# Kernel tuning notes

Hardware: AMD Instinct MI355X
Metric: run time of the kernel (lower is better)

## Reference

```python
import jax, jax.numpy as jnp
import numpy as np

B, Q, K, H = 16, 512, 512, 64
DQ, DK, DV = 256, 256, 256
MASK_VAL = -1000000.0


def setup_inputs() -> dict:
    key = jax.random.key(0)
    ks = jax.random.split(key, 7)
    queries = jax.random.normal(ks[0], (B, Q, DQ), dtype=jnp.float32)
    keys = jax.random.normal(ks[1], (B, K, DK), dtype=jnp.float32)
    values = jax.random.normal(ks[2], (B, K, DV), dtype=jnp.float32)
    valid_lens = jax.random.randint(ks[3], (B,), 1, K + 1).astype(jnp.int32)
    # learned params (nn.Linear, bias=False): weight shape [out, in]
    Wq = jax.random.normal(ks[4], (H, DQ), dtype=jnp.float32) / np.sqrt(DQ)
    Wk = jax.random.normal(ks[5], (H, DK), dtype=jnp.float32) / np.sqrt(DK)
    wv = jax.random.normal(ks[6], (H,), dtype=jnp.float32) / np.sqrt(H)
    return {"queries": queries, "keys": keys, "values": values,
            "valid_lens": valid_lens, "Wq": Wq, "Wk": Wk, "wv": wv}


def reference(queries, keys, values, valid_lens, Wq, Wk, wv):
    q = jnp.einsum('bqd,hd->bqh', queries, Wq)          # [B,Q,H]
    k = jnp.einsum('bkd,hd->bkh', keys, Wk)             # [B,K,H]
    feats = jnp.tanh(q[:, :, None, :] + k[:, None, :, :])  # [B,Q,K,H]
    scores = jnp.einsum('bqkh,h->bqk', feats, wv)       # [B,Q,K]
    kmask = jnp.arange(K)[None, None, :] < valid_lens[:, None, None]
    scores = jnp.where(kmask, scores, MASK_VAL)
    attn = jax.nn.softmax(scores, axis=-1)              # [B,Q,K]
    return jnp.einsum('bqk,bkv->bqv', attn, values)     # [B,Q,DV]
```

## Files before the change

kernel.cpp:

```cpp
#include <hip/hip_runtime.h>
#include <math.h>

#if defined(__has_builtin)
#  if __has_builtin(__builtin_amdgcn_exp2f)
#    define EXP2F(x) __builtin_amdgcn_exp2f(x)
#  endif
#  if __has_builtin(__builtin_amdgcn_rcpf)
#    define RCPF(x) __builtin_amdgcn_rcpf(x)
#  endif
#endif
#ifndef EXP2F
#  define EXP2F(x) exp2f(x)
#endif
#ifndef RCPF
#  define RCPF(x) (1.0f/(x))
#endif

static constexpr int Bn = 16, QN = 512, KN = 512, Hn = 64, DV = 256, DIN = 256;
static constexpr int TQ = 8;
static constexpr float TWO_LOG2E = 2.8853900817779268f;
static constexpr float LOG2E     = 1.4426950408889634f;

__global__ __launch_bounds__(512) void proj_kernel(
    const float* __restrict__ queries, const float* __restrict__ keys,
    const float* __restrict__ Wq, const float* __restrict__ Wk,
    float* __restrict__ qeT, float* __restrict__ ekT)
{
  __shared__ __align__(16) float xs[64][132];
  int t = threadIdx.x;
  int blk = blockIdx.x;
  bool is_k = blk >= 128;
  int tile = blk & 127;
  const float* X = is_k ? keys : queries;
  const float* W = is_k ? Wk : Wq;
  int row0 = tile * 64;
  int lane = t & 63;
  int w8 = __builtin_amdgcn_readfirstlane(t >> 6);
  const float* Wb = W + (size_t)w8 * 8 * DIN;
  float acc[8];
  #pragma unroll
  for (int j = 0; j < 8; ++j) acc[j] = 0.f;

  #pragma unroll
  for (int kc = 0; kc < 2; ++kc) {
    __syncthreads();
    #pragma unroll
    for (int j = 0; j < 4; ++j) {
      int idx = t + 512 * j;
      int row = idx >> 5, c4 = idx & 31;
      *(float4*)&xs[row][c4 * 4] =
          *(const float4*)(X + (size_t)(row0 + row) * DIN + kc * 128 + c4 * 4);
    }
    __syncthreads();
    const float* Wc = Wb + kc * 128;
    #pragma unroll 4
    for (int kq = 0; kq < 32; ++kq) {
      float4 x4 = *(const float4*)&xs[lane][kq * 4];
      #pragma unroll
      for (int j = 0; j < 8; ++j) {
        float4 w4 = *(const float4*)(Wc + j * DIN + kq * 4);
        acc[j] += x4.x * w4.x + x4.y * w4.y + x4.z * w4.z + x4.w * w4.w;
      }
    }
  }
  int row = row0 + lane;
  int b = row >> 9, rk = row & (KN - 1);
  float* outp = is_k ? ekT : qeT;
  #pragma unroll
  for (int j = 0; j < 8; ++j)
    outp[((size_t)b * Hn + w8 * 8 + j) * KN + rk] = EXP2F(acc[j] * TWO_LOG2E);
}

__global__ __launch_bounds__(512) void attn_kernel(
    const float* __restrict__ qeT,
    const float* __restrict__ ekT,
    const float* __restrict__ values,
    const int*   __restrict__ valid_lens,
    const float* __restrict__ wv,
    float* __restrict__ out)
{
  __shared__ __align__(16) float pt[KN][12];
  __shared__ __align__(16) float pacc[3][TQ][DV];
  __shared__ float wsum[8][TQ];
  __shared__ float inv_s[TQ];

  int t = threadIdx.x;
  int b = blockIdx.x >> 6;
  int q0 = (blockIdx.x & 63) * TQ;
  int L = valid_lens[b];
  int lane = t & 63, wave = t >> 6;

  float S = 0.f;
  #pragma unroll
  for (int h = 0; h < Hn; ++h) S += wv[h];

  {
    int k = t;
    float sc[TQ];
    #pragma unroll
    for (int r = 0; r < TQ; ++r) sc[r] = S;
    if (k < L) {
      const float* qbase = qeT + (size_t)b * Hn * QN + q0;
      const float* kbase = ekT + (size_t)b * Hn * KN + k;
      #pragma unroll 2
      for (int h = 0; h < Hn; ++h) {
        float ek = kbase[(size_t)h * KN];
        const float* qp = qbase + (size_t)h * QN;
        float w2 = 2.0f * wv[h];
        #pragma unroll
        for (int r = 0; r < TQ; ++r) {
          float d = qp[r] * ek + 1.0f;
          sc[r] -= w2 * RCPF(d);
        }
      }
    }
    float p[TQ];
    #pragma unroll
    for (int r = 0; r < TQ; ++r) p[r] = (k < L) ? EXP2F(sc[r] * LOG2E) : 0.f;
    if (k < L) {
      *(float4*)&pt[k][0] = make_float4(p[0], p[1], p[2], p[3]);
      *(float4*)&pt[k][4] = make_float4(p[4], p[5], p[6], p[7]);
    }
    #pragma unroll
    for (int r = 0; r < TQ; ++r) {
      float s = p[r];
      #pragma unroll
      for (int off = 32; off > 0; off >>= 1) s += __shfl_xor(s, off, 64);
      if (lane == r) wsum[wave][r] = s;
    }
  }
  __syncthreads();
  if (t < TQ) {
    float s = 0.f;
    #pragma unroll
    for (int w = 0; w < 8; ++w) s += wsum[w][t];
    inv_s[t] = 1.0f / s;
  }
  __syncthreads();

  int p2 = t & 127, kq = t >> 7;
  int c = p2 * 2;
  int k0 = (L * kq) >> 2, k1 = (L * (kq + 1)) >> 2;
  float a0[TQ], a1[TQ];
  #pragma unroll
  for (int r = 0; r < TQ; ++r) { a0[r] = 0.f; a1[r] = 0.f; }
  const float* vb = values + (size_t)b * KN * DV + c;
  #pragma unroll 2
  for (int k = k0; k < k1; ++k) {
    float2 v2 = *(const float2*)(vb + (size_t)k * DV);
    float4 pa = *(const float4*)&pt[k][0];
    float4 pb = *(const float4*)&pt[k][4];
    a0[0] += pa.x * v2.x; a1[0] += pa.x * v2.y;
    a0[1] += pa.y * v2.x; a1[1] += pa.y * v2.y;
    a0[2] += pa.z * v2.x; a1[2] += pa.z * v2.y;
    a0[3] += pa.w * v2.x; a1[3] += pa.w * v2.y;
    a0[4] += pb.x * v2.x; a1[4] += pb.x * v2.y;
    a0[5] += pb.y * v2.x; a1[5] += pb.y * v2.y;
    a0[6] += pb.z * v2.x; a1[6] += pb.z * v2.y;
    a0[7] += pb.w * v2.x; a1[7] += pb.w * v2.y;
  }
  if (kq) {
    #pragma unroll
    for (int r = 0; r < TQ; ++r)
      *(float2*)&pacc[kq - 1][r][c] = make_float2(a0[r], a1[r]);
  }
  __syncthreads();
  if (kq == 0) {
    float* ob = out + ((size_t)b * QN + q0) * DV + c;
    #pragma unroll
    for (int r = 0; r < TQ; ++r) {
      float s0 = a0[r], s1 = a1[r];
      #pragma unroll
      for (int q = 0; q < 3; ++q) {
        float2 pp = *(const float2*)&pacc[q][r][c];
        s0 += pp.x; s1 += pp.y;
      }
      float iv = inv_s[r];
      *(float2*)(ob + (size_t)r * DV) = make_float2(s0 * iv, s1 * iv);
    }
  }
}

extern "C" void kernel_launch(void* const* d_in, const int* in_sizes, int n_in,
                              void* d_out, int out_size, void* d_ws, size_t ws_size,
                              hipStream_t stream) {
  const float* queries    = (const float*)d_in[0];
  const float* keys       = (const float*)d_in[1];
  const float* values     = (const float*)d_in[2];
  const int*   valid_lens = (const int*)d_in[3];
  const float* Wq         = (const float*)d_in[4];
  const float* Wk         = (const float*)d_in[5];
  const float* wv         = (const float*)d_in[6];
  float* out = (float*)d_out;

  float* qeT = (float*)d_ws;
  float* ekT = qeT + (size_t)Bn * Hn * QN;

  proj_kernel<<<256, 512, 0, stream>>>(queries, keys, Wq, Wk, qeT, ekT);
  attn_kernel<<<Bn * (QN / TQ), 512, 0, stream>>>(qeT, ekT, values,
                                                  valid_lens, wv, out);
}
```

Measured before the change: 150.3 us.

## Use MFMA projection and persistent longest-first attention task scheduling

Replaces the scalar projection with a bf16 split-precision (hi/lo three-MFMA) matrix-core kernel that writes queries in row-major layout. Adds an ordering kernel that sorts batches by valid length, and makes the attention kernel persistent, pulling tasks longest-first from an atomic counter to balance the uneven per-batch work. Query features are staged in LDS, and partial outputs are reduced with shared atomics into a single buffer. This adds an extra launch and atomic overhead, and slightly changes projection precision.

```diff
diff --git a/kernel.cpp b/kernel.cpp
--- a/kernel.cpp
+++ b/kernel.cpp
@@ -18,165 +18,231 @@
 
 static constexpr int Bn = 16, QN = 512, KN = 512, Hn = 64, DV = 256, DIN = 256;
 static constexpr int TQ = 8;
+static constexpr int NTASK = Bn * (QN / TQ);
 static constexpr float TWO_LOG2E = 2.8853900817779268f;
 static constexpr float LOG2E     = 1.4426950408889634f;
 
-__global__ __launch_bounds__(512) void proj_kernel(
+typedef __attribute__((ext_vector_type(8))) short short8;
+typedef __attribute__((ext_vector_type(4))) float f32x4;
+
+__device__ __forceinline__ short f2bf(float x) {
+  unsigned u = __builtin_bit_cast(unsigned, x);
+  u += 0x7FFF + ((u >> 16) & 1);
+  return (short)(u >> 16);
+}
+__device__ __forceinline__ float bf2f(short h) {
+  return __builtin_bit_cast(float, ((unsigned)(unsigned short)h) << 16);
+}
+
+__global__ __launch_bounds__(256) void proj_mfma(
     const float* __restrict__ queries, const float* __restrict__ keys,
     const float* __restrict__ Wq, const float* __restrict__ Wk,
-    float* __restrict__ qeT, float* __restrict__ ekT)
+    float* __restrict__ qe, float* __restrict__ ekT)
 {
-  __shared__ __align__(16) float xs[64][132];
   int t = threadIdx.x;
-  int blk = blockIdx.x;
-  bool is_k = blk >= 128;
-  int tile = blk & 127;
+  int lane = t & 63, wid = t >> 6;
+  bool is_k = blockIdx.x >= 128;
   const float* X = is_k ? keys : queries;
   const float* W = is_k ? Wk : Wq;
-  int row0 = tile * 64;
-  int lane = t & 63;
-  int w8 = __builtin_amdgcn_readfirstlane(t >> 6);
-  const float* Wb = W + (size_t)w8 * 8 * DIN;
-  float acc[8];
+  int m0 = (blockIdx.x & 127) * 64 + wid * 16;
+  int mr = lane & 15, quad = lane >> 4;
+  const float* xp = X + (size_t)(m0 + mr) * DIN + quad * 8;
+  const float* wp = W + (size_t)mr * DIN + quad * 8;
+
+  f32x4 acc[4];
   #pragma unroll
-  for (int j = 0; j < 8; ++j) acc[j] = 0.f;
-
+  for (int nt = 0; nt < 4; ++nt) acc[nt] = (f32x4){0.f, 0.f, 0.f, 0.f};
+
+  #pragma unroll 2
+  for (int kc = 0; kc < 8; ++kc) {
+    float4 a0 = *(const float4*)(xp + kc * 32);
+    float4 a1 = *(const float4*)(xp + kc * 32 + 4);
+    float av[8] = {a0.x, a0.y, a0.z, a0.w, a1.x, a1.y, a1.z, a1.w};
+    short8 ah, al;
+    #pragma unroll
+    for (int j = 0; j < 8; ++j) {
+      ah[j] = f2bf(av[j]);
+      al[j] = f2bf(av[j] - bf2f(ah[j]));
+    }
+    #pragma unroll
+    for (int nt = 0; nt < 4; ++nt) {
+      const float* wc = wp + (size_t)nt * 16 * DIN + kc * 32;
+      float4 b0 = *(const float4*)(wc);
+      float4 b1 = *(const float4*)(wc + 4);
+      float bv[8] = {b0.x, b0.y, b0.z, b0.w, b1.x, b1.y, b1.z, b1.w};
+      short8 bh, bl;
+      #pragma unroll
+      for (int j = 0; j < 8; ++j) {
+        bh[j] = f2bf(bv[j]);
+        bl[j] = f2bf(bv[j] - bf2f(bh[j]));
+      }
+      acc[nt] = __builtin_amdgcn_mfma_f32_16x16x32_bf16(al, bh, acc[nt], 0, 0, 0);
+      acc[nt] = __builtin_amdgcn_mfma_f32_16x16x32_bf16(ah, bl, acc[nt], 0, 0, 0);
+      acc[nt] = __builtin_amdgcn_mfma_f32_16x16x32_bf16(ah, bh, acc[nt], 0, 0, 0);
+    }
+  }
   #pragma unroll
-  for (int kc = 0; kc < 2; ++kc) {
-    __syncthreads();
-    #pragma unroll
-    for (int j = 0; j < 4; ++j) {
-      int idx = t + 512 * j;
-      int row = idx >> 5, c4 = idx & 31;
-      *(float4*)&xs[row][c4 * 4] =
-          *(const float4*)(X + (size_t)(row0 + row) * DIN + kc * 128 + c4 * 4);
-    }
-    __syncthreads();
-    const float* Wc = Wb + kc * 128;
-    #pragma unroll 4
-    for (int kq = 0; kq < 32; ++kq) {
-      float4 x4 = *(const float4*)&xs[lane][kq * 4];
-      #pragma unroll
-      for (int j = 0; j < 8; ++j) {
-        float4 w4 = *(const float4*)(Wc + j * DIN + kq * 4);
-        acc[j] += x4.x * w4.x + x4.y * w4.y + x4.z * w4.z + x4.w * w4.w;
-      }
-    }
-  }
-  int row = row0 + lane;
-  int b = row >> 9, rk = row & (KN - 1);
-  float* outp = is_k ? ekT : qeT;
-  #pragma unroll
-  for (int j = 0; j < 8; ++j)
-    outp[((size_t)b * Hn + w8 * 8 + j) * KN + rk] = EXP2F(acc[j] * TWO_LOG2E);
+  for (int nt = 0; nt < 4; ++nt) {
+    int col = nt * 16 + mr;
+    #pragma unroll
+    for (int reg = 0; reg < 4; ++reg) {
+      int row = m0 + quad * 4 + reg;
+      int b = row >> 9, r = row & (QN - 1);
+      float e = EXP2F(acc[nt][reg] * TWO_LOG2E);
+      if (!is_k) qe[((size_t)b * QN + r) * Hn + col] = e;
+      else       ekT[((size_t)b * Hn + col) * KN + r] = e;
+    }
+  }
+}
+
+__global__ void order_kernel(const int* __restrict__ valid_lens,
+                             int* __restrict__ order, int* __restrict__ counter)
+{
+  int t = threadIdx.x;
+  if (t == 0) *counter = 0;
+  __shared__ int batch_at[Bn];
+  if (t < Bn) {
+    int L = valid_lens[t];
+    int r = 0;
+    #pragma unroll
+    for (int b2 = 0; b2 < Bn; ++b2) {
+      int L2 = valid_lens[b2];
+      if (L2 > L || (L2 == L && b2 < t)) ++r;
+    }
+    batch_at[r] = t;
+  }
+  __syncthreads();
+  for (int i = t; i < NTASK; i += 256)
+    order[i] = batch_at[i >> 6] * 64 + (i & 63);
 }
 
 __global__ __launch_bounds__(512) void attn_kernel(
-    const float* __restrict__ qeT,
+    const float* __restrict__ qe,
     const float* __restrict__ ekT,
     const float* __restrict__ values,
     const int*   __restrict__ valid_lens,
     const float* __restrict__ wv,
-    float* __restrict__ out)
+    const int*   __restrict__ order,
+    int*         __restrict__ counter,
+    float*       __restrict__ out)
 {
+  __shared__ __align__(16) float qes2[Hn][8];
   __shared__ __align__(16) float pt[KN][12];
-  __shared__ __align__(16) float pacc[3][TQ][DV];
+  __shared__ __align__(16) float pacc[TQ][DV];
   __shared__ float wsum[8][TQ];
   __shared__ float inv_s[TQ];
+  __shared__ int task_s;
 
   int t = threadIdx.x;
-  int b = blockIdx.x >> 6;
-  int q0 = (blockIdx.x & 63) * TQ;
-  int L = valid_lens[b];
   int lane = t & 63, wave = t >> 6;
 
   float S = 0.f;
   #pragma unroll
   for (int h = 0; h < Hn; ++h) S += wv[h];
 
-  {
-    int k = t;
-    float sc[TQ];
-    #pragma unroll
-    for (int r = 0; r < TQ; ++r) sc[r] = S;
-    if (k < L) {
-      const float* qbase = qeT + (size_t)b * Hn * QN + q0;
-      const float* kbase = ekT + (size_t)b * Hn * KN + k;
-      #pragma unroll 2
-      for (int h = 0; h < Hn; ++h) {
-        float ek = kbase[(size_t)h * KN];
-        const float* qp = qbase + (size_t)h * QN;
-        float w2 = 2.0f * wv[h];
+  while (true) {
+    __syncthreads();
+    if (t == 0) {
+      int ti = atomicAdd(counter, 1);
+      task_s = (ti < NTASK) ? order[ti] : -1;
+    }
+    __syncthreads();
+    int task = task_s;
+    if (task < 0) break;
+    int b = task >> 6, q0 = (task & 63) * TQ;
+    int L = valid_lens[b];
+
+    {
+      int h = t >> 3, r = t & 7;
+      qes2[h][r] = qe[((size_t)b * QN + q0 + r) * Hn + h];
+      #pragma unroll
+      for (int i = t; i < TQ * DV; i += 512) ((float*)pacc)[i] = 0.f;
+    }
+    __syncthreads();
+
+    {
+      int k = t;
+      float sc[TQ];
+      #pragma unroll
+      for (int r = 0; r < TQ; ++r) sc[r] = S;
+      if (k < L) {
+        const float* kbase = ekT + (size_t)b * Hn * KN + k;
+        #pragma unroll 2
+        for (int h = 0; h < Hn; ++h) {
+          float ek = kbase[(size_t)h * KN];
+          float4 qa = *(const float4*)&qes2[h][0];
+          float4 qb = *(const float4*)&qes2[h][4];
+          float w2 = 2.0f * wv[h];
+          sc[0] -= w2 * RCPF(qa.x * ek + 1.0f);
+          sc[1] -= w2 * RCPF(qa.y * ek + 1.0f);
+          sc[2] -= w2 * RCPF(qa.z * ek + 1.0f);
+          sc[3] -= w2 * RCPF(qa.w * ek + 1.0f);
+          sc[4] -= w2 * RCPF(qb.x * ek + 1.0f);
+          sc[5] -= w2 * RCPF(qb.y * ek + 1.0f);
+          sc[6] -= w2 * RCPF(qb.z * ek + 1.0f);
+          sc[7] -= w2 * RCPF(qb.w * ek + 1.0f);
+        }
+      }
+      float p[TQ];
+      #pragma unroll
+      for (int r = 0; r < TQ; ++r) p[r] = (k < L) ? EXP2F(sc[r] * LOG2E) : 0.f;
+      if (k < L) {
+        *(float4*)&pt[k][0] = make_float4(p[0], p[1], p[2], p[3]);
+        *(float4*)&pt[k][4] = make_float4(p[4], p[5], p[6], p[7]);
+      }
+      #pragma unroll
+      for (int r = 0; r < TQ; ++r) {
+        float s = p[r];
         #pragma unroll
-        for (int r = 0; r < TQ; ++r) {
-          float d = qp[r] * ek + 1.0f;
-          sc[r] -= w2 * RCPF(d);
-        }
-      }
-    }
-    float p[TQ];
-    #pragma unroll
-    for (int r = 0; r < TQ; ++r) p[r] = (k < L) ? EXP2F(sc[r] * LOG2E) : 0.f;
-    if (k < L) {
-      *(float4*)&pt[k][0] = make_float4(p[0], p[1], p[2], p[3]);
-      *(float4*)&pt[k][4] = make_float4(p[4], p[5], p[6], p[7]);
-    }
-    #pragma unroll
-    for (int r = 0; r < TQ; ++r) {
-      float s = p[r];
-      #pragma unroll
-      for (int off = 32; off > 0; off >>= 1) s += __shfl_xor(s, off, 64);
-      if (lane == r) wsum[wave][r] = s;
-    }
-  }
-  __syncthreads();
-  if (t < TQ) {
-    float s = 0.f;
-    #pragma unroll
-    for (int w = 0; w < 8; ++w) s += wsum[w][t];
-    inv_s[t] = 1.0f / s;
-  }
-  __syncthreads();
-
-  int p2 = t & 127, kq = t >> 7;
-  int c = p2 * 2;
-  int k0 = (L * kq) >> 2, k1 = (L * (kq + 1)) >> 2;
-  float a0[TQ], a1[TQ];
-  #pragma unroll
-  for (int r = 0; r < TQ; ++r) { a0[r] = 0.f; a1[r] = 0.f; }
-  const float* vb = values + (size_t)b * KN * DV + c;
-  #pragma unroll 2
-  for (int k = k0; k < k1; ++k) {
-    float2 v2 = *(const float2*)(vb + (size_t)k * DV);
-    float4 pa = *(const float4*)&pt[k][0];
-    float4 pb = *(const float4*)&pt[k][4];
-    a0[0] += pa.x * v2.x; a1[0] += pa.x * v2.y;
-    a0[1] += pa.y * v2.x; a1[1] += pa.y * v2.y;
-    a0[2] += pa.z * v2.x; a1[2] += pa.z * v2.y;
-    a0[3] += pa.w * v2.x; a1[3] += pa.w * v2.y;
-    a0[4] += pb.x * v2.x; a1[4] += pb.x * v2.y;
-    a0[5] += pb.y * v2.x; a1[5] += pb.y * v2.y;
-    a0[6] += pb.z * v2.x; a1[6] += pb.z * v2.y;
-    a0[7] += pb.w * v2.x; a1[7] += pb.w * v2.y;
-  }
-  if (kq) {
-    #pragma unroll
-    for (int r = 0; r < TQ; ++r)
-      *(float2*)&pacc[kq - 1][r][c] = make_float2(a0[r], a1[r]);
-  }
-  __syncthreads();
-  if (kq == 0) {
-    float* ob = out + ((size_t)b * QN + q0) * DV + c;
-    #pragma unroll
-    for (int r = 0; r < TQ; ++r) {
-      float s0 = a0[r], s1 = a1[r];
-      #pragma unroll
-      for (int q = 0; q < 3; ++q) {
-        float2 pp = *(const float2*)&pacc[q][r][c];
-        s0 += pp.x; s1 += pp.y;
-      }
-      float iv = inv_s[r];
-      *(float2*)(ob + (size_t)r * DV) = make_float2(s0 * iv, s1 * iv);
+        for (int off = 32; off > 0; off >>= 1) s += __shfl_xor(s, off, 64);
+        if (lane == r) wsum[wave][r] = s;
+      }
+    }
+    __syncthreads();
+    if (t < TQ) {
+      float s = 0.f;
+      #pragma unroll
+      for (int w = 0; w < 8; ++w) s += wsum[w][t];
+      inv_s[t] = 1.0f / s;
+    }
+
+    int p2 = t & 127, kq = t >> 7;
+    int c = p2 * 2;
+    int k0 = (L * kq) >> 2, k1 = (L * (kq + 1)) >> 2;
+    float a0[TQ], a1[TQ];
+    #pragma unroll
+    for (int r = 0; r < TQ; ++r) { a0[r] = 0.f; a1[r] = 0.f; }
+    const float* vb = values + (size_t)b * KN * DV + c;
+    #pragma unroll 2
+    for (int k = k0; k < k1; ++k) {
+      float2 v2 = *(const float2*)(vb + (size_t)k * DV);
+      float4 pa = *(const float4*)&pt[k][0];
+      float4 pb = *(const float4*)&pt[k][4];
+      a0[0] += pa.x * v2.x; a1[0] += pa.x * v2.y;
+      a0[1] += pa.y * v2.x; a1[1] += pa.y * v2.y;
+      a0[2] += pa.z * v2.x; a1[2] += pa.z * v2.y;
+      a0[3] += pa.w * v2.x; a1[3] += pa.w * v2.y;
+      a0[4] += pb.x * v2.x; a1[4] += pb.x * v2.y;
+      a0[5] += pb.y * v2.x; a1[5] += pb.y * v2.y;
+      a0[6] += pb.z * v2.x; a1[6] += pb.z * v2.y;
+      a0[7] += pb.w * v2.x; a1[7] += pb.w * v2.y;
+    }
+    if (kq) {
+      #pragma unroll
+      for (int r = 0; r < TQ; ++r) {
+        atomicAdd(&pacc[r][c],     a0[r]);
+        atomicAdd(&pacc[r][c + 1], a1[r]);
+      }
+    }
+    __syncthreads();
+    if (kq == 0) {
+      float* ob = out + ((size_t)b * QN + q0) * DV + c;
+      #pragma unroll
+      for (int r = 0; r < TQ; ++r) {
+        float iv = inv_s[r];
+        *(float2*)(ob + (size_t)r * DV) =
+            make_float2((a0[r] + pacc[r][c]) * iv, (a1[r] + pacc[r][c + 1]) * iv);
+      }
     }
   }
 }
@@ -193,10 +259,14 @@
   const float* wv         = (const float*)d_in[6];
   float* out = (float*)d_out;
 
-  float* qeT = (float*)d_ws;
-  float* ekT = qeT + (size_t)Bn * Hn * QN;
-
-  proj_kernel<<<256, 512, 0, stream>>>(queries, keys, Wq, Wk, qeT, ekT);
-  attn_kernel<<<Bn * (QN / TQ), 512, 0, stream>>>(qeT, ekT, values,
-                                                  valid_lens, wv, out);
-}
+  char* ws = (char*)d_ws;
+  int*   order   = (int*)ws;
+  int*   counter = (int*)(ws + 4096);
+  float* qe      = (float*)(ws + 8192);
+  float* ekT     = qe + (size_t)Bn * QN * Hn;
+
+  proj_mfma<<<256, 256, 0, stream>>>(queries, keys, Wq, Wk, qe, ekT);
+  order_kernel<<<1, 256, 0, stream>>>(valid_lens, order, counter);
+  attn_kernel<<<768, 512, 0, stream>>>(qe, ekT, values, valid_lens, wv,
+                                       order, counter, out);
+}
```

Measured after the change: 184.7 us. 1.23x slower.

## Use split-bf16 MFMA projection and load-balance attention blocks by valid length

Applied to the files above, without the earlier changes.

Replaces the FP32 projection with a 3-pass split-bf16 MFMA GEMM, fed by a new prep kernel that splits the weights into high and low bf16 parts. The attention kernel now gives each block two (batch, query-tile) tasks, pairing long and short valid lengths by rank to balance work. It also stages query features in shared memory and pairs heads to share one reciprocal per two tanh terms. The intent is to cut projection cost and tail imbalance from variable valid_lens. In exchange it adds a third launch, halves the block count, and accepts small precision loss from the bf16 split and the merged reciprocal.

```diff
diff --git a/kernel.cpp b/kernel.cpp
--- a/kernel.cpp
+++ b/kernel.cpp
@@ -21,163 +21,241 @@
 static constexpr float TWO_LOG2E = 2.8853900817779268f;
 static constexpr float LOG2E     = 1.4426950408889634f;
 
-__global__ __launch_bounds__(512) void proj_kernel(
+typedef __attribute__((ext_vector_type(8))) short short8;
+typedef __attribute__((ext_vector_type(4))) float f32x4;
+
+__device__ __forceinline__ short f2bf(float x) {
+  unsigned u = __builtin_bit_cast(unsigned, x);
+  u += 0x7FFF + ((u >> 16) & 1);
+  return (short)(u >> 16);
+}
+__device__ __forceinline__ float bf2f(short h) {
+  return __builtin_bit_cast(float, ((unsigned)(unsigned short)h) << 16);
+}
+
+__global__ __launch_bounds__(256) void prep_kernel(
+    const float* __restrict__ Wq, const float* __restrict__ Wk,
+    ushort* __restrict__ wqh, ushort* __restrict__ wql,
+    ushort* __restrict__ wkh, ushort* __restrict__ wkl)
+{
+  int i = blockIdx.x * 256 + threadIdx.x;
+  float xq = Wq[i];
+  short hq = f2bf(xq);
+  wqh[i] = (ushort)hq; wql[i] = (ushort)f2bf(xq - bf2f(hq));
+  float xk = Wk[i];
+  short hk = f2bf(xk);
+  wkh[i] = (ushort)hk; wkl[i] = (ushort)f2bf(xk - bf2f(hk));
+}
+
+__global__ __launch_bounds__(256) void proj_mfma(
     const float* __restrict__ queries, const float* __restrict__ keys,
-    const float* __restrict__ Wq, const float* __restrict__ Wk,
-    float* __restrict__ qeT, float* __restrict__ ekT)
+    const ushort* __restrict__ wqh, const ushort* __restrict__ wql,
+    const ushort* __restrict__ wkh, const ushort* __restrict__ wkl,
+    float* __restrict__ qe, float* __restrict__ ekT)
 {
-  __shared__ __align__(16) float xs[64][132];
+  __shared__ float tr[4][16][20];
   int t = threadIdx.x;
-  int blk = blockIdx.x;
-  bool is_k = blk >= 128;
-  int tile = blk & 127;
-  const float* X = is_k ? keys : queries;
-  const float* W = is_k ? Wk : Wq;
-  int row0 = tile * 64;
-  int lane = t & 63;
-  int w8 = __builtin_amdgcn_readfirstlane(t >> 6);
-  const float* Wb = W + (size_t)w8 * 8 * DIN;
-  float acc[8];
+  int lane = t & 63, wid = t >> 6;
+  bool is_k = blockIdx.x >= 512;
+  int trow = (blockIdx.x & 511) * 16;
+  const float*  X  = is_k ? keys : queries;
+  const ushort* Wh = is_k ? wkh : wqh;
+  const ushort* Wl = is_k ? wkl : wql;
+  int mr = lane & 15, quad = lane >> 4;
+  const float*  xp  = X  + (size_t)(trow + mr) * DIN + quad * 8;
+  const ushort* whp = Wh + (size_t)(wid * 16 + mr) * DIN + quad * 8;
+  const ushort* wlp = Wl + (size_t)(wid * 16 + mr) * DIN + quad * 8;
+
+  f32x4 acc = (f32x4){0.f, 0.f, 0.f, 0.f};
   #pragma unroll
-  for (int j = 0; j < 8; ++j) acc[j] = 0.f;
-
-  #pragma unroll
-  for (int kc = 0; kc < 2; ++kc) {
-    __syncthreads();
-    #pragma unroll
-    for (int j = 0; j < 4; ++j) {
-      int idx = t + 512 * j;
-      int row = idx >> 5, c4 = idx & 31;
-      *(float4*)&xs[row][c4 * 4] =
-          *(const float4*)(X + (size_t)(row0 + row) * DIN + kc * 128 + c4 * 4);
-    }
-    __syncthreads();
-    const float* Wc = Wb + kc * 128;
-    #pragma unroll 4
-    for (int kq = 0; kq < 32; ++kq) {
-      float4 x4 = *(const float4*)&xs[lane][kq * 4];
-      #pragma unroll
-      for (int j = 0; j < 8; ++j) {
-        float4 w4 = *(const float4*)(Wc + j * DIN + kq * 4);
-        acc[j] += x4.x * w4.x + x4.y * w4.y + x4.z * w4.z + x4.w * w4.w;
-      }
-    }
-  }
-  int row = row0 + lane;
-  int b = row >> 9, rk = row & (KN - 1);
-  float* outp = is_k ? ekT : qeT;
-  #pragma unroll
-  for (int j = 0; j < 8; ++j)
-    outp[((size_t)b * Hn + w8 * 8 + j) * KN + rk] = EXP2F(acc[j] * TWO_LOG2E);
+  for (int kc = 0; kc < 8; ++kc) {
+    float4 a0 = *(const float4*)(xp + kc * 32);
+    float4 a1 = *(const float4*)(xp + kc * 32 + 4);
+    float av[8] = {a0.x, a0.y, a0.z, a0.w, a1.x, a1.y, a1.z, a1.w};
+    short8 ah, al;
+    #pragma unroll
+    for (int j = 0; j < 8; ++j) {
+      ah[j] = f2bf(av[j]);
+      al[j] = f2bf(av[j] - bf2f(ah[j]));
+    }
+    short8 bh = *(const short8*)(whp + kc * 32);
+    short8 bl = *(const short8*)(wlp + kc * 32);
+    acc = __builtin_amdgcn_mfma_f32_16x16x32_bf16(al, bh, acc, 0, 0, 0);
+    acc = __builtin_amdgcn_mfma_f32_16x16x32_bf16(ah, bl, acc, 0, 0, 0);
+    acc = __builtin_amdgcn_mfma_f32_16x16x32_bf16(ah, bh, acc, 0, 0, 0);
+  }
+  if (!is_k) {
+    #pragma unroll
+    for (int reg = 0; reg < 4; ++reg) {
+      int row = trow + quad * 4 + reg;
+      qe[(size_t)row * Hn + wid * 16 + mr] = EXP2F(acc[reg] * TWO_LOG2E);
+    }
+  } else {
+    #pragma unroll
+    for (int reg = 0; reg < 4; ++reg)
+      tr[wid][mr][quad * 4 + reg] = EXP2F(acc[reg] * TWO_LOG2E);
+    int b = trow >> 9, kr = trow & (KN - 1);
+    #pragma unroll
+    for (int hp = 0; hp < 4; ++hp) {
+      int h_l = hp * 4 + quad, k_l = mr;
+      ekT[((size_t)b * Hn + wid * 16 + h_l) * KN + kr + k_l] = tr[wid][h_l][k_l];
+    }
+  }
 }
 
 __global__ __launch_bounds__(512) void attn_kernel(
-    const float* __restrict__ qeT,
+    const float* __restrict__ qe,
     const float* __restrict__ ekT,
     const float* __restrict__ values,
     const int*   __restrict__ valid_lens,
     const float* __restrict__ wv,
     float* __restrict__ out)
 {
+  __shared__ __align__(16) float qes2[Hn][TQ];
   __shared__ __align__(16) float pt[KN][12];
   __shared__ __align__(16) float pacc[3][TQ][DV];
   __shared__ float wsum[8][TQ];
   __shared__ float inv_s[TQ];
 
   int t = threadIdx.x;
-  int b = blockIdx.x >> 6;
-  int q0 = (blockIdx.x & 63) * TQ;
-  int L = valid_lens[b];
   int lane = t & 63, wave = t >> 6;
+
+  int iA = blockIdx.x, iB = 1023 - blockIdx.x;
+  int rankA = iA >> 6, rankB = iB >> 6;
+  int bA = 0, bB = 0;
+  for (int bb = 0; bb < Bn; ++bb) {
+    int Lb = valid_lens[bb];
+    int r = 0;
+    for (int b2 = 0; b2 < Bn; ++b2) {
+      int L2 = valid_lens[b2];
+      r += (L2 > Lb || (L2 == Lb && b2 < bb)) ? 1 : 0;
+    }
+    if (r == rankA) bA = bb;
+    if (r == rankB) bB = bb;
+  }
+  int tb[2] = {bA, bB};
+  int tq[2] = {(iA & 63) * TQ, (iB & 63) * TQ};
 
   float S = 0.f;
   #pragma unroll
   for (int h = 0; h < Hn; ++h) S += wv[h];
 
-  {
-    int k = t;
-    float sc[TQ];
-    #pragma unroll
-    for (int r = 0; r < TQ; ++r) sc[r] = S;
-    if (k < L) {
-      const float* qbase = qeT + (size_t)b * Hn * QN + q0;
-      const float* kbase = ekT + (size_t)b * Hn * KN + k;
-      #pragma unroll 2
-      for (int h = 0; h < Hn; ++h) {
-        float ek = kbase[(size_t)h * KN];
-        const float* qp = qbase + (size_t)h * QN;
-        float w2 = 2.0f * wv[h];
-        #pragma unroll
-        for (int r = 0; r < TQ; ++r) {
-          float d = qp[r] * ek + 1.0f;
-          sc[r] -= w2 * RCPF(d);
+  for (int ti = 0; ti < 2; ++ti) {
+    int b = tb[ti], q0 = tq[ti];
+    int L = valid_lens[b];
+
+    qes2[t >> 3][t & 7] = qe[(size_t)(b * QN + q0 + (t & 7)) * Hn + (t >> 3)];
+    __syncthreads();
+
+    {
+      int k = t;
+      float p[TQ];
+      if (k < L) {
+        float sc[TQ];
+        #pragma unroll
+        for (int r = 0; r < TQ; ++r) sc[r] = S;
+        const float* kb = ekT + (size_t)b * Hn * KN + k;
+        for (int h0 = 0; h0 < Hn; h0 += 8) {
+          float ekv[8];
+          #pragma unroll
+          for (int j = 0; j < 8; ++j)
+            ekv[j] = kb[(size_t)(h0 + j) * KN];
+          #pragma unroll
+          for (int jp = 0; jp < 4; ++jp) {
+            int ha = h0 + 2 * jp;
+            float wa = 2.0f * wv[ha], wb = 2.0f * wv[ha + 1];
+            float eka = ekv[2 * jp], ekb = ekv[2 * jp + 1];
+            float4 qa0 = *(const float4*)&qes2[ha][0];
+            float4 qa1 = *(const float4*)&qes2[ha][4];
+            float4 qb0 = *(const float4*)&qes2[ha + 1][0];
+            float4 qb1 = *(const float4*)&qes2[ha + 1][4];
+            {
+              float da, db, num;
+              da = qa0.x * eka + 1.0f; db = qb0.x * ekb + 1.0f;
+              num = wa * db + wb * da; sc[0] -= num * RCPF(da * db);
+              da = qa0.y * eka + 1.0f; db = qb0.y * ekb + 1.0f;
+              num = wa * db + wb * da; sc[1] -= num * RCPF(da * db);
+              da = qa0.z * eka + 1.0f; db = qb0.z * ekb + 1.0f;
+              num = wa * db + wb * da; sc[2] -= num * RCPF(da * db);
+              da = qa0.w * eka + 1.0f; db = qb0.w * ekb + 1.0f;
+              num = wa * db + wb * da; sc[3] -= num * RCPF(da * db);
+              da = qa1.x * eka + 1.0f; db = qb1.x * ekb + 1.0f;
+              num = wa * db + wb * da; sc[4] -= num * RCPF(da * db);
+              da = qa1.y * eka + 1.0f; db = qb1.y * ekb + 1.0f;
+              num = wa * db + wb * da; sc[5] -= num * RCPF(da * db);
+              da = qa1.z * eka + 1.0f; db = qb1.z * ekb + 1.0f;
+              num = wa * db + wb * da; sc[6] -= num * RCPF(da * db);
+              da = qa1.w * eka + 1.0f; db = qb1.w * ekb + 1.0f;
+              num = wa * db + wb * da; sc[7] -= num * RCPF(da * db);
+            }
+          }
         }
+        #pragma unroll
+        for (int r = 0; r < TQ; ++r) p[r] = EXP2F(sc[r] * LOG2E);
+        *(float4*)&pt[k][0] = make_float4(p[0], p[1], p[2], p[3]);
+        *(float4*)&pt[k][4] = make_float4(p[4], p[5], p[6], p[7]);
+      } else {
+        #pragma unroll
+        for (int r = 0; r < TQ; ++r) p[r] = 0.f;
       }
-    }
-    float p[TQ];
-    #pragma unroll
-    for (int r = 0; r < TQ; ++r) p[r] = (k < L) ? EXP2F(sc[r] * LOG2E) : 0.f;
-    if (k < L) {
-      *(float4*)&pt[k][0] = make_float4(p[0], p[1], p[2], p[3]);
-      *(float4*)&pt[k][4] = make_float4(p[4], p[5], p[6], p[7]);
-    }
-    #pragma unroll
-    for (int r = 0; r < TQ; ++r) {
-      float s = p[r];
-      #pragma unroll
-      for (int off = 32; off > 0; off >>= 1) s += __shfl_xor(s, off, 64);
-      if (lane == r) wsum[wave][r] = s;
-    }
-  }
-  __syncthreads();
-  if (t < TQ) {
-    float s = 0.f;
-    #pragma unroll
-    for (int w = 0; w < 8; ++w) s += wsum[w][t];
-    inv_s[t] = 1.0f / s;
-  }
-  __syncthreads();
-
-  int p2 = t & 127, kq = t >> 7;
-  int c = p2 * 2;
-  int k0 = (L * kq) >> 2, k1 = (L * (kq + 1)) >> 2;
-  float a0[TQ], a1[TQ];
-  #pragma unroll
-  for (int r = 0; r < TQ; ++r) { a0[r] = 0.f; a1[r] = 0.f; }
-  const float* vb = values + (size_t)b * KN * DV + c;
-  #pragma unroll 2
-  for (int k = k0; k < k1; ++k) {
-    float2 v2 = *(const float2*)(vb + (size_t)k * DV);
-    float4 pa = *(const float4*)&pt[k][0];
-    float4 pb = *(const float4*)&pt[k][4];
-    a0[0] += pa.x * v2.x; a1[0] += pa.x * v2.y;
-    a0[1] += pa.y * v2.x; a1[1] += pa.y * v2.y;
-    a0[2] += pa.z * v2.x; a1[2] += pa.z * v2.y;
-    a0[3] += pa.w * v2.x; a1[3] += pa.w * v2.y;
-    a0[4] += pb.x * v2.x; a1[4] += pb.x * v2.y;
-    a0[5] += pb.y * v2.x; a1[5] += pb.y * v2.y;
-    a0[6] += pb.z * v2.x; a1[6] += pb.z * v2.y;
-    a0[7] += pb.w * v2.x; a1[7] += pb.w * v2.y;
-  }
-  if (kq) {
-    #pragma unroll
-    for (int r = 0; r < TQ; ++r)
-      *(float2*)&pacc[kq - 1][r][c] = make_float2(a0[r], a1[r]);
-  }
-  __syncthreads();
-  if (kq == 0) {
-    float* ob = out + ((size_t)b * QN + q0) * DV + c;
-    #pragma unroll
-    for (int r = 0; r < TQ; ++r) {
-      float s0 = a0[r], s1 = a1[r];
-      #pragma unroll
-      for (int q = 0; q < 3; ++q) {
-        float2 pp = *(const float2*)&pacc[q][r][c];
-        s0 += pp.x; s1 += pp.y;
+      #pragma unroll
+      for (int r = 0; r < TQ; ++r) {
+        float s = p[r];
+        #pragma unroll
+        for (int off = 32; off > 0; off >>= 1) s += __shfl_xor(s, off, 64);
+        if (lane == r) wsum[wave][r] = s;
       }
-      float iv = inv_s[r];
-      *(float2*)(ob + (size_t)r * DV) = make_float2(s0 * iv, s1 * iv);
-    }
+    }
+    __syncthreads();
+    if (t < TQ) {
+      float s = 0.f;
+      #pragma unroll
+      for (int w = 0; w < 8; ++w) s += wsum[w][t];
+      inv_s[t] = 1.0f / s;
+    }
+
+    int cp = t & 127, kq = t >> 7;
+    int c = 2 * cp;
+    int k0 = (L * kq) >> 2, k1 = (L * (kq + 1)) >> 2;
+    float a0[TQ], a1[TQ];
+    #pragma unroll
+    for (int r = 0; r < TQ; ++r) { a0[r] = 0.f; a1[r] = 0.f; }
+    const float* vb = values + (size_t)b * KN * DV + c;
+    #pragma unroll 2
+    for (int k = k0; k < k1; ++k) {
+      float2 v2 = *(const float2*)(vb + (size_t)k * DV);
+      float4 pa = *(const float4*)&pt[k][0];
+      float4 pb = *(const float4*)&pt[k][4];
+      a0[0] += pa.x * v2.x; a1[0] += pa.x * v2.y;
+      a0[1] += pa.y * v2.x; a1[1] += pa.y * v2.y;
+      a0[2] += pa.z * v2.x; a1[2] += pa.z * v2.y;
+      a0[3] += pa.w * v2.x; a1[3] += pa.w * v2.y;
+      a0[4] += pb.x * v2.x; a1[4] += pb.x * v2.y;
+      a0[5] += pb.y * v2.x; a1[5] += pb.y * v2.y;
+      a0[6] += pb.z * v2.x; a1[6] += pb.z * v2.y;
+      a0[7] += pb.w * v2.x; a1[7] += pb.w * v2.y;
+    }
+    if (kq) {
+      #pragma unroll
+      for (int r = 0; r < TQ; ++r)
+        *(float2*)&pacc[kq - 1][r][c] = make_float2(a0[r], a1[r]);
+    }
+    __syncthreads();
+    if (kq == 0) {
+      float* ob = out + (size_t)(b * QN + q0) * DV + c;
+      #pragma unroll
+      for (int r = 0; r < TQ; ++r) {
+        float s0 = a0[r], s1 = a1[r];
+        #pragma unroll
+        for (int q = 0; q < 3; ++q) {
+          float2 pp = *(const float2*)&pacc[q][r][c];
+          s0 += pp.x; s1 += pp.y;
+        }
+        float iv = inv_s[r];
+        *(float2*)(ob + (size_t)r * DV) = make_float2(s0 * iv, s1 * iv);
+      }
+    }
+    __syncthreads();
   }
 }
 
@@ -193,10 +271,15 @@
   const float* wv         = (const float*)d_in[6];
   float* out = (float*)d_out;
 
-  float* qeT = (float*)d_ws;
-  float* ekT = qeT + (size_t)Bn * Hn * QN;
-
-  proj_kernel<<<256, 512, 0, stream>>>(queries, keys, Wq, Wk, qeT, ekT);
-  attn_kernel<<<Bn * (QN / TQ), 512, 0, stream>>>(qeT, ekT, values,
-                                                  valid_lens, wv, out);
-}
+  char* ws = (char*)d_ws;
+  float*  qe  = (float*)ws;
+  float*  ekT = qe + (size_t)Bn * QN * Hn;
+  ushort* wqh = (ushort*)(ekT + (size_t)Bn * Hn * KN);
+  ushort* wql = wqh + Hn * DIN;
+  ushort* wkh = wql + Hn * DIN;
+  ushort* wkl = wkh + Hn * DIN;
+
+  prep_kernel<<<64, 256, 0, stream>>>(Wq, Wk, wqh, wql, wkh, wkl);
+  proj_mfma<<<1024, 256, 0, stream>>>(queries, keys, wqh, wql, wkh, wkl, qe, ekT);
+  attn_kernel<<<512, 512, 0, stream>>>(qe, ekT, values, valid_lens, wv, out);
+}
```

Result: no change. 152.8 us (+1.7%).
